# Optimization experiments

Measured on AMD Instinct MI355X. Metric: run time of the kernel, lower is better.

Reference implementation:

```python
import jax, jax.numpy as jnp
import numpy as np

B, N, D = 64, 512, 128  # graphs per batch, max nodes per graph, hidden_dim


def setup_inputs() -> dict:
    key = jax.random.key(0)
    ks = jax.random.split(key, 9)
    h1 = jax.random.normal(ks[0], (B, N, D), jnp.float32)
    h2 = jax.random.normal(ks[1], (B, N, D), jnp.float32)
    s = 1.0 / np.sqrt(D)
    Wk = jax.random.normal(ks[2], (D, D), jnp.float32) * s
    bk = jax.random.normal(ks[3], (D,), jnp.float32) * s
    Wq = jax.random.normal(ks[4], (D, D), jnp.float32) * s
    bq = jax.random.normal(ks[5], (D,), jnp.float32) * s
    t = jnp.asarray(np.sqrt(1.0 / D), jnp.float32)  # self.t = sqrt(1/hidden_dim)
    len1 = jax.random.randint(ks[6], (B,), 1, N + 1, jnp.int32)
    len2 = jax.random.randint(ks[7], (B,), 1, N + 1, jnp.int32)
    return {"h1": h1, "h2": h2, "Wk": Wk, "bk": bk, "Wq": Wq, "bq": bq,
            "t": t, "len1": len1, "len2": len2}


def reference(h1, h2, Wk, bk, Wq, bq, t, len1, len2):
    # valid-node masks for the ragged (padded) graphs
    pos = jnp.arange(N)
    m1 = pos[None, :] < len1[:, None]  # [B, N]
    m2 = pos[None, :] < len2[:, None]  # [B, N]

    # k = Linear(h), q = Linear(h)  (torch Linear: x @ W.T + b)
    k1 = jnp.einsum('bnd,ed->bne', h1, Wk) + bk
    k2 = jnp.einsum('bnd,ed->bne', h2, Wk) + bk
    q1 = jnp.einsum('bnd,ed->bne', h1, Wq) + bq
    q2 = jnp.einsum('bnd,ed->bne', h2, Wq) + bq

    NEG = jnp.asarray(-1e9, h1.dtype)

    # g1 nodes attend over g2 nodes; note values == keys (k2)
    s1 = jnp.einsum('bnd,bmd->bnm', q1, k2) * t           # [B, N1, N2]
    s1 = jnp.where(m2[:, None, :], s1, NEG)
    a1 = jax.nn.softmax(s1, axis=-1)
    o1 = jnp.einsum('bnm,bmd->bnd', a1, k2) * m1[:, :, None]

    # g2 nodes attend over g1 nodes; values == k1
    s2 = jnp.einsum('bnd,bmd->bnm', q2, k1) * t           # [B, N2, N1]
    s2 = jnp.where(m1[:, None, :], s2, NEG)
    a2 = jax.nn.softmax(s2, axis=-1)
    o2 = jnp.einsum('bnm,bmd->bnd', a2, k1) * m2[:, :, None]

    return o1, o2
```

## Files before the change

kernel.cpp:

```cpp
#include <hip/hip_runtime.h>

typedef __attribute__((ext_vector_type(8))) short bf16x8;
typedef __attribute__((ext_vector_type(4))) short s16x4;
typedef __attribute__((ext_vector_type(4))) float f32x4;
typedef __attribute__((ext_vector_type(4))) int   i32x4;

#define MFMA16 __builtin_amdgcn_mfma_f32_16x16x32_bf16

#define B_ 64
#define N_ 512
#define D_ 128

__device__ __forceinline__ unsigned short f2bf(float f) {
  unsigned u = __builtin_bit_cast(unsigned, f);
  u += 0x7fffu + ((u >> 16) & 1u);
  return (unsigned short)(u >> 16);
}
__device__ __forceinline__ int packbf2(float lo, float hi) {
  return (int)((unsigned)f2bf(lo) | ((unsigned)f2bf(hi) << 16));
}

__device__ __forceinline__ void gload_lds16(const void* g, void* l) {
  __builtin_amdgcn_global_load_lds((const __attribute__((address_space(1))) unsigned*)g,
                                   (__attribute__((address_space(3))) unsigned*)l, 16, 0, 0);
}

__global__ void prep_w(const float* __restrict__ Wk, const float* __restrict__ Wq,
                       short* __restrict__ wkb, short* __restrict__ wqb) {
  int i = blockIdx.x * 256 + threadIdx.x;
  if (i < D_ * D_) { wkb[i] = (short)f2bf(Wk[i]); wqb[i] = (short)f2bf(Wq[i]); }
}

__global__ __launch_bounds__(256, 2) void proj_kernel(
    const float* __restrict__ h1, const float* __restrict__ h2,
    const short* __restrict__ wkb, const short* __restrict__ wqb,
    const float* __restrict__ bk, const float* __restrict__ bq,
    short* __restrict__ k1, short* __restrict__ k2,
    short* __restrict__ q1, short* __restrict__ q2,
    short* __restrict__ k1T, short* __restrict__ k2T) {
  const int wave = threadIdx.x >> 6, lane = threadIdx.x & 63;
  const int c = lane & 15, g = lane >> 4;
  const int rw = blockIdx.x * 128 + wave * 32;
  const int inp = rw >> 15;
  const int loc = rw & 32767;
  const int b = loc >> 9, n0 = loc & 511;
  const float* __restrict__ h = inp ? h2 : h1;
  short* __restrict__ kout = inp ? k2 : k1;
  short* __restrict__ qout = inp ? q2 : q1;
  short* __restrict__ kT   = inp ? k2T : k1T;

  bf16x8 xf[2][4];
#pragma unroll
  for (int mt = 0; mt < 2; ++mt) {
    const float* hr = h + (long)(loc + mt * 16 + c) * D_;
#pragma unroll
    for (int kk = 0; kk < 4; ++kk) {
      f32x4 lo = *(const f32x4*)(hr + kk * 32 + g * 8);
      f32x4 hi = *(const f32x4*)(hr + kk * 32 + g * 8 + 4);
      bf16x8 v;
      v[0] = (short)f2bf(lo[0]); v[1] = (short)f2bf(lo[1]);
      v[2] = (short)f2bf(lo[2]); v[3] = (short)f2bf(lo[3]);
      v[4] = (short)f2bf(hi[0]); v[5] = (short)f2bf(hi[1]);
      v[6] = (short)f2bf(hi[2]); v[7] = (short)f2bf(hi[3]);
      xf[mt][kk] = v;
    }
  }

#pragma unroll
  for (int et = 0; et < 8; ++et) {
    bf16x8 wkf[4], wqf[4];
    const short* wkr = wkb + (et * 16 + c) * D_;
    const short* wqr = wqb + (et * 16 + c) * D_;
#pragma unroll
    for (int kk = 0; kk < 4; ++kk) {
      wkf[kk] = *(const bf16x8*)(wkr + kk * 32 + g * 8);
      wqf[kk] = *(const bf16x8*)(wqr + kk * 32 + g * 8);
    }
    f32x4 ak[2], aq[2], at[2];
#pragma unroll
    for (int mt = 0; mt < 2; ++mt) {
      ak[mt] = (f32x4){0.f, 0.f, 0.f, 0.f};
      aq[mt] = (f32x4){0.f, 0.f, 0.f, 0.f};
      at[mt] = (f32x4){0.f, 0.f, 0.f, 0.f};
    }
#pragma unroll
    for (int kk = 0; kk < 4; ++kk) {
#pragma unroll
      for (int mt = 0; mt < 2; ++mt) {
        ak[mt] = MFMA16(wkf[kk], xf[mt][kk], ak[mt], 0, 0, 0);
        aq[mt] = MFMA16(wqf[kk], xf[mt][kk], aq[mt], 0, 0, 0);
        at[mt] = MFMA16(xf[mt][kk], wkf[kk], at[mt], 0, 0, 0);
      }
    }
    f32x4 bkv = *(const f32x4*)(bk + et * 16 + g * 4);
    f32x4 bqv = *(const f32x4*)(bq + et * 16 + g * 4);
    float bks = bk[et * 16 + c];
#pragma unroll
    for (int mt = 0; mt < 2; ++mt) {
      s16x4 pk, pq, pt;
#pragma unroll
      for (int j = 0; j < 4; ++j) {
        pk[j] = (short)f2bf(ak[mt][j] + bkv[j]);
        pq[j] = (short)f2bf(aq[mt][j] + bqv[j]);
        pt[j] = (short)f2bf(at[mt][j] + bks);
      }
      long row = (long)(loc + mt * 16 + c);
      *(s16x4*)(kout + row * D_ + et * 16 + g * 4) = pk;
      *(s16x4*)(qout + row * D_ + et * 16 + g * 4) = pq;
      *(s16x4*)(kT + ((long)(b * D_ + et * 16 + c)) * N_ + n0 + mt * 16 + g * 4) = pt;
    }
  }
}

#define CH_ 64
#define NCH_ (N_ / CH_)
#define KBUF_ 16384

__global__ __launch_bounds__(256, 2) void attn_kernel(
    const short* __restrict__ k1, const short* __restrict__ k2,
    const short* __restrict__ q1, const short* __restrict__ q2,
    const short* __restrict__ k1T, const short* __restrict__ k2T,
    const float* __restrict__ tptr,
    const int* __restrict__ len1, const int* __restrict__ len2,
    float* __restrict__ out) {
  extern __shared__ char smem[];
  const int tid = threadIdx.x;
  const int wave = tid >> 6, lane = tid & 63;
  const int c = lane & 15, g = lane >> 4;
  const int qt = blockIdx.x, b = blockIdx.y, dir = blockIdx.z;
  const short* __restrict__ qp = dir ? q2 : q1;
  const short* __restrict__ kp = dir ? k1 : k2;
  const short* __restrict__ vT = dir ? k1T : k2T;
  const int lk = dir ? len1[b] : len2[b];
  const int lq = dir ? len2[b] : len1[b];
  float* __restrict__ o = out + (long)dir * B_ * N_ * D_;
  const float ts = *tptr;
  const int q0 = qt * 64 + wave * 16;

  const char* kbase = (const char*)(kp + (long)b * N_ * D_);
  const char* vbase = (const char*)(vT + (long)b * D_ * N_);

  auto stage_k = [&](int ch, char* buf) {
#pragma unroll
    for (int i = 0; i < 4; ++i) {
      int L = i * 4096 + tid * 16;
      int row = L >> 8, off = L & 255;
      int srco = off ^ ((row & 7) << 4);
      const char* gp = kbase + (ch * 64 + row) * 256 + srco;
      char* lp = buf + i * 4096 + (wave << 10);
      gload_lds16(gp, lp);
    }
  };
  auto stage_v = [&](int ch, char* buf) {
#pragma unroll
    for (int i = 0; i < 4; ++i) {
      int L = i * 4096 + tid * 16;
      int row = L >> 7, off = L & 127;
      int srco = off ^ ((row & 7) << 4);
      const char* gp = vbase + row * 1024 + ch * 128 + srco;
      char* lp = buf + i * 4096 + (wave << 10);
      gload_lds16(gp, lp);
    }
  };

  bf16x8 qf[4];
  const short* qrow = qp + ((long)(b * N_ + q0 + c)) * D_;
#pragma unroll
  for (int kk = 0; kk < 4; ++kk) qf[kk] = *(const bf16x8*)(qrow + kk * 32 + g * 8);

  f32x4 s[32];
  stage_k(0, smem);
  __syncthreads();
#pragma unroll
  for (int ch = 0; ch < NCH_; ++ch) {
    if (ch + 1 < NCH_) stage_k(ch + 1, smem + KBUF_ * ((ch + 1) & 1));
    const char* buf = smem + KBUF_ * (ch & 1);
#pragma unroll
    for (int tl = 0; tl < 4; ++tl) {
      int r = tl * 16 + c;
      const char* base = buf + (r << 8);
      int sw = (r & 7) << 4;
      f32x4 acc = (f32x4){0.f, 0.f, 0.f, 0.f};
#pragma unroll
      for (int kk = 0; kk < 4; ++kk) {
        bf16x8 kf = *(const bf16x8*)(base + ((kk * 64 + g * 16) ^ sw));
        acc = MFMA16(kf, qf[kk], acc, 0, 0, 0);
      }
      const int node = ch * 64 + tl * 16 + g * 4;
#pragma unroll
      for (int j = 0; j < 4; ++j) {
        float v = acc[j] * ts;
        s[ch * 4 + tl][j] = (node + j < lk) ? v : -1e9f;
      }
    }
    __syncthreads();
  }

  stage_v(0, smem);

  float mx = -3e38f;
#pragma unroll
  for (int t16 = 0; t16 < 32; ++t16)
#pragma unroll
    for (int j = 0; j < 4; ++j) mx = fmaxf(mx, s[t16][j]);
  mx = fmaxf(mx, __shfl_xor(mx, 16));
  mx = fmaxf(mx, __shfl_xor(mx, 32));
  float rs = 0.f;
#pragma unroll
  for (int t16 = 0; t16 < 32; ++t16)
#pragma unroll
    for (int j = 0; j < 4; ++j) {
      float p = __expf(s[t16][j] - mx);
      s[t16][j] = p;
      rs += p;
    }
  rs += __shfl_xor(rs, 16);
  rs += __shfl_xor(rs, 32);
  const float rinv = 1.0f / rs;
  __syncthreads();

  f32x4 oacc[8];
#pragma unroll
  for (int dt = 0; dt < 8; ++dt) oacc[dt] = (f32x4){0.f, 0.f, 0.f, 0.f};
  const int srcA = c + ((g & 1) << 5);
  const int srcB = srcA + 16;
  const bool lowhalf = (g < 2);
#pragma unroll
  for (int ch = 0; ch < NCH_; ++ch) {
    if (ch + 1 < NCH_) stage_v(ch + 1, smem + KBUF_ * ((ch + 1) & 1));
    const char* buf = smem + KBUF_ * (ch & 1);
#pragma unroll
    for (int q = 0; q < 2; ++q) {
      int t0 = ch * 4 + 2 * q;
      int a0 = packbf2(s[t0][0], s[t0][1]);
      int a1 = packbf2(s[t0][2], s[t0][3]);
      int b0 = packbf2(s[t0 + 1][0], s[t0 + 1][1]);
      int b1 = packbf2(s[t0 + 1][2], s[t0 + 1][3]);
      int xa0 = __shfl(a0, srcA), xb0 = __shfl(b0, srcA);
      int xa1 = __shfl(a1, srcA), xb1 = __shfl(b1, srcA);
      int ya0 = __shfl(a0, srcB), yb0 = __shfl(b0, srcB);
      int ya1 = __shfl(a1, srcB), yb1 = __shfl(b1, srcB);
      i32x4 ui;
      ui[0] = lowhalf ? xa0 : xb0;
      ui[1] = lowhalf ? xa1 : xb1;
      ui[2] = lowhalf ? ya0 : yb0;
      ui[3] = lowhalf ? ya1 : yb1;
      bf16x8 pf = __builtin_bit_cast(bf16x8, ui);
#pragma unroll
      for (int dt = 0; dt < 8; ++dt) {
        int row = dt * 16 + c;
        bf16x8 vt = *(const bf16x8*)(buf + row * 128 + ((q * 64 + g * 16) ^ ((row & 7) << 4)));
        oacc[dt] = MFMA16(vt, pf, oacc[dt], 0, 0, 0);
      }
    }
    __syncthreads();
  }

  const int qg = q0 + c;
  const bool valid = qg < lq;
  float* orow = o + ((long)(b * N_ + qg)) * D_;
#pragma unroll
  for (int dt = 0; dt < 8; ++dt) {
    f32x4 vo;
#pragma unroll
    for (int j = 0; j < 4; ++j) vo[j] = valid ? oacc[dt][j] * rinv : 0.0f;
    *(f32x4*)(orow + dt * 16 + g * 4) = vo;
  }
}

extern "C" void kernel_launch(void* const* d_in, const int* in_sizes, int n_in,
                              void* d_out, int out_size, void* d_ws, size_t ws_size,
                              hipStream_t stream) {
  const float* h1 = (const float*)d_in[0];
  const float* h2 = (const float*)d_in[1];
  const float* Wk = (const float*)d_in[2];
  const float* bk = (const float*)d_in[3];
  const float* Wq = (const float*)d_in[4];
  const float* bq = (const float*)d_in[5];
  const float* t  = (const float*)d_in[6];
  const int* len1 = (const int*)d_in[7];
  const int* len2 = (const int*)d_in[8];

  char* ws = (char*)d_ws;
  const size_t SZ = (size_t)B_ * N_ * D_ * 2;
  short* k1  = (short*)(ws + 0 * SZ);
  short* k2  = (short*)(ws + 1 * SZ);
  short* q1  = (short*)(ws + 2 * SZ);
  short* q2  = (short*)(ws + 3 * SZ);
  short* k1T = (short*)(ws + 4 * SZ);
  short* k2T = (short*)(ws + 5 * SZ);
  short* wkb = (short*)(ws + 6 * SZ);
  short* wqb = (short*)(ws + 6 * SZ + D_ * D_ * 2);

  prep_w<<<64, 256, 0, stream>>>(Wk, Wq, wkb, wqb);
  proj_kernel<<<512, 256, 0, stream>>>(h1, h2, wkb, wqb, bk, bq,
                                       k1, k2, q1, q2, k1T, k2T);
  attn_kernel<<<dim3(8, 64, 2), 256, 2 * KBUF_, stream>>>(k1, k2, q1, q2, k1T, k2T,
                                                          t, len1, len2, (float*)d_out);
}
```

Before: 84.98 us.

## Triple-buffer K/V staging as one 16-stage stream with single barrier per chunk

Merges the K and V chunk loads into one unified 16-step pipeline over three LDS buffers with prefetch depth two. Each chunk now needs one barrier (vmcnt wait plus s_barrier) instead of two __syncthreads, and the V prefetch starts during the K phase. It also adds s_setprio around the MFMA sections and flattens the grid so that consecutive workgroups cover different batches and directions for the same query tile. LDS use rises from 32KB to 48KB per block, which could limit occupancy, and the hand-written vmcnt counts must match the number of loads issued.

```diff
diff --git a/kernel.cpp b/kernel.cpp
--- a/kernel.cpp
+++ b/kernel.cpp
@@ -10,6 +10,7 @@
 #define B_ 64
 #define N_ 512
 #define D_ 128
+#define KBUF_ 16384
 
 __device__ __forceinline__ unsigned short f2bf(float f) {
   unsigned u = __builtin_bit_cast(unsigned, f);
@@ -112,10 +113,6 @@
   }
 }
 
-#define CH_ 64
-#define NCH_ (N_ / CH_)
-#define KBUF_ 16384
-
 __global__ __launch_bounds__(256, 2) void attn_kernel(
     const short* __restrict__ k1, const short* __restrict__ k2,
     const short* __restrict__ q1, const short* __restrict__ q2,
@@ -127,7 +124,10 @@
   const int tid = threadIdx.x;
   const int wave = tid >> 6, lane = tid & 63;
   const int c = lane & 15, g = lane >> 4;
-  const int qt = blockIdx.x, b = blockIdx.y, dir = blockIdx.z;
+  const int wgid = blockIdx.x;
+  const int qt = wgid >> 7;
+  const int bd = wgid & 127;
+  const int dir = bd >> 6, b = bd & 63;
   const short* __restrict__ qp = dir ? q2 : q1;
   const short* __restrict__ kp = dir ? k1 : k2;
   const short* __restrict__ vT = dir ? k1T : k2T;
@@ -140,26 +140,25 @@
   const char* kbase = (const char*)(kp + (long)b * N_ * D_);
   const char* vbase = (const char*)(vT + (long)b * D_ * N_);
 
-  auto stage_k = [&](int ch, char* buf) {
-#pragma unroll
-    for (int i = 0; i < 4; ++i) {
-      int L = i * 4096 + tid * 16;
-      int row = L >> 8, off = L & 255;
-      int srco = off ^ ((row & 7) << 4);
-      const char* gp = kbase + (ch * 64 + row) * 256 + srco;
-      char* lp = buf + i * 4096 + (wave << 10);
-      gload_lds16(gp, lp);
-    }
-  };
-  auto stage_v = [&](int ch, char* buf) {
-#pragma unroll
-    for (int i = 0; i < 4; ++i) {
-      int L = i * 4096 + tid * 16;
-      int row = L >> 7, off = L & 127;
-      int srco = off ^ ((row & 7) << 4);
-      const char* gp = vbase + row * 1024 + ch * 128 + srco;
-      char* lp = buf + i * 4096 + (wave << 10);
-      gload_lds16(gp, lp);
+  auto stage = [&](int i) {
+    char* buf = smem + KBUF_ * (i % 3);
+    if (i < 8) {
+#pragma unroll
+      for (int j = 0; j < 4; ++j) {
+        int L = j * 4096 + tid * 16;
+        int row = L >> 8, off = L & 255;
+        const char* gp = kbase + (i * 64 + row) * 256 + (off ^ ((row & 7) << 4));
+        gload_lds16(gp, buf + j * 4096 + (wave << 10));
+      }
+    } else {
+      int ch = i - 8;
+#pragma unroll
+      for (int j = 0; j < 4; ++j) {
+        int L = j * 4096 + tid * 16;
+        int row = L >> 7, off = L & 127;
+        const char* gp = vbase + row * 1024 + ch * 128 + (off ^ ((row & 7) << 4));
+        gload_lds16(gp, buf + j * 4096 + (wave << 10));
+      }
     }
   };
 
@@ -168,13 +167,19 @@
 #pragma unroll
   for (int kk = 0; kk < 4; ++kk) qf[kk] = *(const bf16x8*)(qrow + kk * 32 + g * 8);
 
+  stage(0);
+  stage(1);
+
   f32x4 s[32];
-  stage_k(0, smem);
-  __syncthreads();
-#pragma unroll
-  for (int ch = 0; ch < NCH_; ++ch) {
-    if (ch + 1 < NCH_) stage_k(ch + 1, smem + KBUF_ * ((ch + 1) & 1));
-    const char* buf = smem + KBUF_ * (ch & 1);
+#pragma unroll
+  for (int ch = 0; ch < 8; ++ch) {
+    asm volatile("s_waitcnt vmcnt(4)" ::: "memory");
+    __builtin_amdgcn_sched_barrier(0);
+    __builtin_amdgcn_s_barrier();
+    __builtin_amdgcn_sched_barrier(0);
+    stage(ch + 2);
+    const char* buf = smem + KBUF_ * (ch % 3);
+    __builtin_amdgcn_s_setprio(1);
 #pragma unroll
     for (int tl = 0; tl < 4; ++tl) {
       int r = tl * 16 + c;
@@ -193,10 +198,8 @@
         s[ch * 4 + tl][j] = (node + j < lk) ? v : -1e9f;
       }
     }
-    __syncthreads();
-  }
-
-  stage_v(0, smem);
+    __builtin_amdgcn_s_setprio(0);
+  }
 
   float mx = -3e38f;
 #pragma unroll
@@ -217,7 +220,6 @@
   rs += __shfl_xor(rs, 16);
   rs += __shfl_xor(rs, 32);
   const float rinv = 1.0f / rs;
-  __syncthreads();
 
   f32x4 oacc[8];
 #pragma unroll
@@ -226,9 +228,14 @@
   const int srcB = srcA + 16;
   const bool lowhalf = (g < 2);
 #pragma unroll
-  for (int ch = 0; ch < NCH_; ++ch) {
-    if (ch + 1 < NCH_) stage_v(ch + 1, smem + KBUF_ * ((ch + 1) & 1));
-    const char* buf = smem + KBUF_ * (ch & 1);
+  for (int ch = 0; ch < 8; ++ch) {
+    if (ch == 7) asm volatile("s_waitcnt vmcnt(0)" ::: "memory");
+    else         asm volatile("s_waitcnt vmcnt(4)" ::: "memory");
+    __builtin_amdgcn_sched_barrier(0);
+    __builtin_amdgcn_s_barrier();
+    __builtin_amdgcn_sched_barrier(0);
+    if (ch + 10 < 16) stage(ch + 10);
+    const char* buf = smem + KBUF_ * ((ch + 8) % 3);
 #pragma unroll
     for (int q = 0; q < 2; ++q) {
       int t0 = ch * 4 + 2 * q;
@@ -246,14 +253,15 @@
       ui[2] = lowhalf ? ya0 : yb0;
       ui[3] = lowhalf ? ya1 : yb1;
       bf16x8 pf = __builtin_bit_cast(bf16x8, ui);
+      __builtin_amdgcn_s_setprio(1);
 #pragma unroll
       for (int dt = 0; dt < 8; ++dt) {
         int row = dt * 16 + c;
         bf16x8 vt = *(const bf16x8*)(buf + row * 128 + ((q * 64 + g * 16) ^ ((row & 7) << 4)));
         oacc[dt] = MFMA16(vt, pf, oacc[dt], 0, 0, 0);
       }
-    }
-    __syncthreads();
+      __builtin_amdgcn_s_setprio(0);
+    }
   }
 
   const int qg = q0 + c;
@@ -295,6 +303,6 @@
   prep_w<<<64, 256, 0, stream>>>(Wk, Wq, wkb, wqb);
   proj_kernel<<<512, 256, 0, stream>>>(h1, h2, wkb, wqb, bk, bq,
                                        k1, k2, q1, q2, k1T, k2T);
-  attn_kernel<<<dim3(8, 64, 2), 256, 2 * KBUF_, stream>>>(k1, k2, q1, q2, k1T, k2T,
-                                                          t, len1, len2, (float*)d_out);
-}
+  attn_kernel<<<1024, 256, 3 * KBUF_, stream>>>(k1, k2, q1, q2, k1T, k2T,
+                                                t, len1, len2, (float*)d_out);
+}
```

New measurement: 75.94 us. 1.12x faster.
